# Optimization experiments

Hardware: AMD Instinct MI355X
Metric: run time of the kernel (lower is better)

## Reference

```python
import jax, jax.numpy as jnp
import numpy as np

B, T, D, HD = 256, 256, 384, 64  # batch, seq_len, embedding_dim, head_dim


def setup_inputs() -> dict:
    key = jax.random.key(0)
    k1, k2, k3, k4 = jax.random.split(key, 4)
    x = jax.random.normal(k1, (B, T, D), dtype=jnp.float32)
    # nn.Linear(D, HD, bias=False) weight shape is [HD, D]; init scaled like kaiming-uniform magnitude
    Wq = jax.random.normal(k2, (HD, D), dtype=jnp.float32) * (1.0 / np.sqrt(D))
    Wk = jax.random.normal(k3, (HD, D), dtype=jnp.float32) * (1.0 / np.sqrt(D))
    Wv = jax.random.normal(k4, (HD, D), dtype=jnp.float32) * (1.0 / np.sqrt(D))
    return {"x": x, "Wq": Wq, "Wk": Wk, "Wv": Wv}


def reference(x, Wq, Wk, Wv):
    # Projections: x @ W^T  (Linear with bias=False)
    q = jnp.einsum('btd,hd->bth', x, Wq)  # [B,T,HD]
    k = jnp.einsum('btd,hd->bth', x, Wk)
    v = jnp.einsum('btd,hd->bth', x, Wv)
    scale = 1.0 / np.sqrt(HD).astype(np.float32)
    scores = jnp.einsum('bqh,bkh->bqk', q, k) * scale  # [B,T,T]
    T_ = x.shape[1]
    causal = jnp.tril(jnp.ones((T_, T_), dtype=bool))
    scores = jnp.where(causal, scores, jnp.float32(-jnp.inf))
    attn = jax.nn.softmax(scores, axis=-1)
    # dropout disabled (eval mode) for deterministic reference
    return jnp.einsum('bqk,bkh->bqh', attn, v)
```

## Files before the change

### kernel.cpp

```cpp
#include <hip/hip_runtime.h>

typedef __attribute__((ext_vector_type(8))) short bf16x8;
typedef __attribute__((ext_vector_type(4))) float f32x4;

__device__ inline unsigned short f2bf(float f) {
    unsigned u = __float_as_uint(f);
    return (unsigned short)((u + 0x7fffu + ((u >> 16) & 1u)) >> 16);
}

__global__ void wconv(const float* __restrict__ Wq, const float* __restrict__ Wk,
                      const float* __restrict__ Wv, short* __restrict__ Wcat) {
    int i = blockIdx.x * 256 + threadIdx.x;
    if (i >= 192 * 384) return;
    int row = i / 384;
    int col = i - row * 384;
    const float* src = row < 64 ? (Wq + row * 384)
                     : row < 128 ? (Wk + (row - 64) * 384)
                                 : (Wv + (row - 128) * 384);
    Wcat[i] = (short)f2bf(src[col]);
}

__global__ __launch_bounds__(256) void qkv_proj_mfma(
    const float* __restrict__ x, const short* __restrict__ Wcat,
    short* __restrict__ Qw, short* __restrict__ Kw, short* __restrict__ Vw) {
    __shared__ short xs[128 * 72];
    __shared__ short wsh[192 * 72];
    const int tid = threadIdx.x;
    const int wv = tid >> 6, lane = tid & 63;
    const int g = lane >> 4, c = lane & 15;
    const int wm = (wv >> 1) * 64, wn = (wv & 1) * 96;
    const long long m0 = (long long)blockIdx.x * 128;

    f32x4 acc[4][6];
#pragma unroll
    for (int i = 0; i < 4; ++i)
#pragma unroll
        for (int j = 0; j < 6; ++j) acc[i][j] = (f32x4){0.f, 0.f, 0.f, 0.f};

    for (int kc = 0; kc < 6; ++kc) {
#pragma unroll
        for (int p = 0; p < 8; ++p) {
            int r = p * 16 + (tid >> 4);
            int c4 = tid & 15;
            float4 v = *(const float4*)(x + (m0 + r) * 384 + kc * 64 + c4 * 4);
            unsigned lo = (unsigned)f2bf(v.x) | ((unsigned)f2bf(v.y) << 16);
            unsigned hi = (unsigned)f2bf(v.z) | ((unsigned)f2bf(v.w) << 16);
            *(uint2*)&xs[r * 72 + c4 * 4] = make_uint2(lo, hi);
        }
#pragma unroll
        for (int p = 0; p < 12; ++p) {
            int idx = tid + 256 * p;
            int r = idx >> 4;
            int c2 = idx & 15;
            uint2 w2 = *(const uint2*)(Wcat + r * 384 + kc * 64 + c2 * 4);
            *(uint2*)&wsh[r * 72 + c2 * 4] = w2;
        }
        __syncthreads();
#pragma unroll
        for (int ks = 0; ks < 2; ++ks) {
            bf16x8 af[4], bfr[6];
#pragma unroll
            for (int mi = 0; mi < 4; ++mi)
                af[mi] = *(const bf16x8*)&xs[(wm + 16 * mi + c) * 72 + ks * 32 + g * 8];
#pragma unroll
            for (int nj = 0; nj < 6; ++nj)
                bfr[nj] = *(const bf16x8*)&wsh[(wn + 16 * nj + c) * 72 + ks * 32 + g * 8];
#pragma unroll
            for (int mi = 0; mi < 4; ++mi)
#pragma unroll
                for (int nj = 0; nj < 6; ++nj)
                    acc[mi][nj] = __builtin_amdgcn_mfma_f32_16x16x32_bf16(
                        af[mi], bfr[nj], acc[mi][nj], 0, 0, 0);
        }
        __syncthreads();
    }
#pragma unroll
    for (int mi = 0; mi < 4; ++mi) {
#pragma unroll
        for (int nj = 0; nj < 6; ++nj) {
            int colb = wn + 16 * nj;
            short* dst = colb < 64 ? Qw : (colb < 128 ? Kw : Vw);
            int hc = (colb & 63) + c;
#pragma unroll
            for (int r = 0; r < 4; ++r) {
                long long row = m0 + wm + 16 * mi + 4 * g + r;
                dst[row * 64 + hc] = (short)f2bf(acc[mi][nj][r]);
            }
        }
    }
}

__global__ __launch_bounds__(512) void attn_mfma(
    const short* __restrict__ Qw, const short* __restrict__ Kw,
    const short* __restrict__ Vw, float* __restrict__ out) {
    __shared__ short Ksh[256 * 72];
    __shared__ short Vt[64 * 264];
    __shared__ short Pb[8][16 * 40];
    const int tid = threadIdx.x;
    const int wv = tid >> 6, lane = tid & 63;
    const int g = lane >> 4, c = lane & 15;
    const int b = blockIdx.x;
    const short* Qg = Qw + b * 16384;
    const short* Kg = Kw + b * 16384;
    const short* Vg = Vw + b * 16384;

#pragma unroll
    for (int p = 0; p < 4; ++p) {
        int idx = tid + 512 * p;
        int r = idx >> 3, q8 = idx & 7;
        *(uint4*)&Ksh[r * 72 + q8 * 8] = *(const uint4*)(Kg + r * 64 + q8 * 8);
    }
#pragma unroll
    for (int p = 0; p < 4; ++p) {
        int idx = tid + 512 * p;
        int r = idx >> 3, q8 = idx & 7;
        uint4 v = *(const uint4*)(Vg + r * 64 + q8 * 8);
        unsigned vw[4] = {v.x, v.y, v.z, v.w};
        int swz = (q8 & 7) << 3;
#pragma unroll
        for (int w2 = 0; w2 < 4; ++w2) {
            int h0 = q8 * 8 + w2 * 2;
            Vt[((h0 + 0) * 264 + r) ^ swz] = (short)(vw[w2] & 0xffff);
            Vt[((h0 + 1) * 264 + r) ^ swz] = (short)(vw[w2] >> 16);
        }
    }
    __syncthreads();

    for (int half = 0; half < 2; ++half) {
        const int q0 = (half == 0) ? 16 * wv : 240 - 16 * wv;
        bf16x8 qf0 = *(const bf16x8*)(Qg + (q0 + c) * 64 + g * 8);
        bf16x8 qf1 = *(const bf16x8*)(Qg + (q0 + c) * 64 + 32 + g * 8);
        f32x4 o[4];
#pragma unroll
        for (int nj = 0; nj < 4; ++nj) o[nj] = (f32x4){0.f, 0.f, 0.f, 0.f};
        float m[4] = {-INFINITY, -INFINITY, -INFINITY, -INFINITY};
        float ls[4] = {0.f, 0.f, 0.f, 0.f};
        const int jmax = (q0 + 15) >> 5;

        for (int j = 0; j <= jmax; ++j) {
            f32x4 s0 = {0.f, 0.f, 0.f, 0.f}, s1 = {0.f, 0.f, 0.f, 0.f};
            {
                bf16x8 kf;
                kf = *(const bf16x8*)&Ksh[(32 * j + c) * 72 + g * 8];
                s0 = __builtin_amdgcn_mfma_f32_16x16x32_bf16(qf0, kf, s0, 0, 0, 0);
                kf = *(const bf16x8*)&Ksh[(32 * j + c) * 72 + 32 + g * 8];
                s0 = __builtin_amdgcn_mfma_f32_16x16x32_bf16(qf1, kf, s0, 0, 0, 0);
                kf = *(const bf16x8*)&Ksh[(32 * j + 16 + c) * 72 + g * 8];
                s1 = __builtin_amdgcn_mfma_f32_16x16x32_bf16(qf0, kf, s1, 0, 0, 0);
                kf = *(const bf16x8*)&Ksh[(32 * j + 16 + c) * 72 + 32 + g * 8];
                s1 = __builtin_amdgcn_mfma_f32_16x16x32_bf16(qf1, kf, s1, 0, 0, 0);
            }
            float t0[4], t1[4];
#pragma unroll
            for (int r = 0; r < 4; ++r) {
                t0[r] = s0[r] * 0.125f;
                t1[r] = s1[r] * 0.125f;
            }
            if (j == jmax) {
                int q = q0 + 4 * g;
#pragma unroll
                for (int r = 0; r < 4; ++r) {
                    if (32 * j + c > q + r) t0[r] = -INFINITY;
                    if (32 * j + 16 + c > q + r) t1[r] = -INFINITY;
                }
            }
            float corr[4], p0[4], p1[4];
#pragma unroll
            for (int r = 0; r < 4; ++r) {
                float v = fmaxf(t0[r], t1[r]);
#pragma unroll
                for (int off = 1; off < 16; off <<= 1) v = fmaxf(v, __shfl_xor(v, off, 16));
                float mn = fmaxf(m[r], v);
                corr[r] = __expf(m[r] - mn);
                m[r] = mn;
                p0[r] = __expf(t0[r] - mn);
                p1[r] = __expf(t1[r] - mn);
                float rs = p0[r] + p1[r];
#pragma unroll
                for (int off = 1; off < 16; off <<= 1) rs += __shfl_xor(rs, off, 16);
                ls[r] = ls[r] * corr[r] + rs;
            }
#pragma unroll
            for (int nj = 0; nj < 4; ++nj) {
                f32x4 t = o[nj];
                t[0] *= corr[0]; t[1] *= corr[1]; t[2] *= corr[2]; t[3] *= corr[3];
                o[nj] = t;
            }
            short* pb = Pb[wv];
#pragma unroll
            for (int r = 0; r < 4; ++r) {
                pb[(4 * g + r) * 40 + c]      = (short)f2bf(p0[r]);
                pb[(4 * g + r) * 40 + 16 + c] = (short)f2bf(p1[r]);
            }
            bf16x8 pa = *(const bf16x8*)&pb[c * 40 + g * 8];
#pragma unroll
            for (int nj = 0; nj < 4; ++nj) {
                int h = 16 * nj + c;
                int swz = ((2 * nj + (c >> 3)) & 7) << 3;
                bf16x8 vf = *(const bf16x8*)&Vt[(h * 264 + 32 * j + g * 8) ^ swz];
                o[nj] = __builtin_amdgcn_mfma_f32_16x16x32_bf16(pa, vf, o[nj], 0, 0, 0);
            }
        }
        float inv[4];
#pragma unroll
        for (int r = 0; r < 4; ++r) inv[r] = 1.f / ls[r];
        float* ob = out + ((size_t)b * 256 + q0) * 64;
#pragma unroll
        for (int nj = 0; nj < 4; ++nj)
#pragma unroll
            for (int r = 0; r < 4; ++r)
                ob[(4 * g + r) * 64 + 16 * nj + c] = o[nj][r] * inv[r];
    }
}

extern "C" void kernel_launch(void* const* d_in, const int* in_sizes, int n_in,
                              void* d_out, int out_size, void* d_ws, size_t ws_size,
                              hipStream_t stream) {
    const float* x  = (const float*)d_in[0];
    const float* Wq = (const float*)d_in[1];
    const float* Wk = (const float*)d_in[2];
    const float* Wv = (const float*)d_in[3];
    float* out = (float*)d_out;

    short* Qws  = (short*)d_ws;
    short* Kws  = Qws + (size_t)65536 * 64;
    short* Vws  = Kws + (size_t)65536 * 64;
    short* Wcat = Vws + (size_t)65536 * 64;

    wconv<<<dim3(288), dim3(256), 0, stream>>>(Wq, Wk, Wv, Wcat);
    qkv_proj_mfma<<<dim3(512), dim3(256), 0, stream>>>(x, Wcat, Qws, Kws, Vws);
    attn_mfma<<<dim3(256), dim3(512), 0, stream>>>(Qws, Kws, Vws, out);
}
```

Baseline: 50.76 us.

## Fuse QKV projection into attention kernel, keeping Q/K/V in LDS

Merges the projection GEMM and the attention kernel into one per-batch kernel. Each block computes its 256x192 QKV tile with MFMA, reading x and weight fragments straight from global memory with register prefetch, then writes Q, K and a transposed V into shared memory before running attention. This removes the global round trip for Q/K/V and one kernel launch. In exchange each block does 256 rows of projection with 8 waves, LDS use rises (which may limit occupancy), and the weights are reread per block without LDS staging.

New measurement: 62.75 us. 1.24x slower.

```diff
diff --git a/kernel.cpp b/kernel.cpp
--- a/kernel.cpp
+++ b/kernel.cpp
@@ -20,16 +20,28 @@
     Wcat[i] = (short)f2bf(src[col]);
 }
 
-__global__ __launch_bounds__(256) void qkv_proj_mfma(
+__global__ __launch_bounds__(512, 2) void fused_attn(
     const float* __restrict__ x, const short* __restrict__ Wcat,
-    short* __restrict__ Qw, short* __restrict__ Kw, short* __restrict__ Vw) {
-    __shared__ short xs[128 * 72];
-    __shared__ short wsh[192 * 72];
+    float* __restrict__ out) {
+    __shared__ short Qlds[256 * 72];
+    __shared__ short Ksh[256 * 72];
+    __shared__ short Vt[64 * 264];
+    __shared__ short Pb[8][16 * 40];
+
     const int tid = threadIdx.x;
     const int wv = tid >> 6, lane = tid & 63;
     const int g = lane >> 4, c = lane & 15;
     const int wm = (wv >> 1) * 64, wn = (wv & 1) * 96;
-    const long long m0 = (long long)blockIdx.x * 128;
+    const int b = blockIdx.x;
+
+    const float* xA[4];
+#pragma unroll
+    for (int mi = 0; mi < 4; ++mi)
+        xA[mi] = x + ((size_t)b * 256 + wm + 16 * mi + c) * 384 + g * 8;
+    const short* Bp[6];
+#pragma unroll
+    for (int nj = 0; nj < 6; ++nj)
+        Bp[nj] = Wcat + (wn + 16 * nj + c) * 384 + g * 8;
 
     f32x4 acc[4][6];
 #pragma unroll
@@ -37,99 +49,77 @@
 #pragma unroll
         for (int j = 0; j < 6; ++j) acc[i][j] = (f32x4){0.f, 0.f, 0.f, 0.f};
 
-    for (int kc = 0; kc < 6; ++kc) {
-#pragma unroll
-        for (int p = 0; p < 8; ++p) {
-            int r = p * 16 + (tid >> 4);
-            int c4 = tid & 15;
-            float4 v = *(const float4*)(x + (m0 + r) * 384 + kc * 64 + c4 * 4);
-            unsigned lo = (unsigned)f2bf(v.x) | ((unsigned)f2bf(v.y) << 16);
-            unsigned hi = (unsigned)f2bf(v.z) | ((unsigned)f2bf(v.w) << 16);
-            *(uint2*)&xs[r * 72 + c4 * 4] = make_uint2(lo, hi);
-        }
-#pragma unroll
-        for (int p = 0; p < 12; ++p) {
-            int idx = tid + 256 * p;
-            int r = idx >> 4;
-            int c2 = idx & 15;
-            uint2 w2 = *(const uint2*)(Wcat + r * 384 + kc * 64 + c2 * 4);
-            *(uint2*)&wsh[r * 72 + c2 * 4] = w2;
-        }
-        __syncthreads();
-#pragma unroll
-        for (int ks = 0; ks < 2; ++ks) {
-            bf16x8 af[4], bfr[6];
-#pragma unroll
-            for (int mi = 0; mi < 4; ++mi)
-                af[mi] = *(const bf16x8*)&xs[(wm + 16 * mi + c) * 72 + ks * 32 + g * 8];
+    float4 pa[4][2];
+#pragma unroll
+    for (int mi = 0; mi < 4; ++mi) {
+        pa[mi][0] = *(const float4*)(xA[mi] + 0);
+        pa[mi][1] = *(const float4*)(xA[mi] + 4);
+    }
+
+    for (int s = 0; s < 12; ++s) {
+        const int kn = (s < 11 ? s + 1 : 11) * 32;
+        float4 na[4][2];
+#pragma unroll
+        for (int mi = 0; mi < 4; ++mi) {
+            na[mi][0] = *(const float4*)(xA[mi] + kn + 0);
+            na[mi][1] = *(const float4*)(xA[mi] + kn + 4);
+        }
+        bf16x8 bfr[6];
+#pragma unroll
+        for (int nj = 0; nj < 6; ++nj)
+            bfr[nj] = *(const bf16x8*)(Bp[nj] + s * 32);
+        bf16x8 af[4];
+#pragma unroll
+        for (int mi = 0; mi < 4; ++mi) {
+            bf16x8 t;
+            t[0] = (short)f2bf(pa[mi][0].x); t[1] = (short)f2bf(pa[mi][0].y);
+            t[2] = (short)f2bf(pa[mi][0].z); t[3] = (short)f2bf(pa[mi][0].w);
+            t[4] = (short)f2bf(pa[mi][1].x); t[5] = (short)f2bf(pa[mi][1].y);
+            t[6] = (short)f2bf(pa[mi][1].z); t[7] = (short)f2bf(pa[mi][1].w);
+            af[mi] = t;
+        }
+#pragma unroll
+        for (int mi = 0; mi < 4; ++mi)
 #pragma unroll
             for (int nj = 0; nj < 6; ++nj)
-                bfr[nj] = *(const bf16x8*)&wsh[(wn + 16 * nj + c) * 72 + ks * 32 + g * 8];
-#pragma unroll
-            for (int mi = 0; mi < 4; ++mi)
-#pragma unroll
-                for (int nj = 0; nj < 6; ++nj)
-                    acc[mi][nj] = __builtin_amdgcn_mfma_f32_16x16x32_bf16(
-                        af[mi], bfr[nj], acc[mi][nj], 0, 0, 0);
-        }
-        __syncthreads();
-    }
+                acc[mi][nj] = __builtin_amdgcn_mfma_f32_16x16x32_bf16(
+                    af[mi], bfr[nj], acc[mi][nj], 0, 0, 0);
+#pragma unroll
+        for (int mi = 0; mi < 4; ++mi) {
+            pa[mi][0] = na[mi][0];
+            pa[mi][1] = na[mi][1];
+        }
+    }
+
 #pragma unroll
     for (int mi = 0; mi < 4; ++mi) {
 #pragma unroll
         for (int nj = 0; nj < 6; ++nj) {
-            int colb = wn + 16 * nj;
-            short* dst = colb < 64 ? Qw : (colb < 128 ? Kw : Vw);
-            int hc = (colb & 63) + c;
-#pragma unroll
-            for (int r = 0; r < 4; ++r) {
-                long long row = m0 + wm + 16 * mi + 4 * g + r;
-                dst[row * 64 + hc] = (short)f2bf(acc[mi][nj][r]);
-            }
-        }
-    }
-}
-
-__global__ __launch_bounds__(512) void attn_mfma(
-    const short* __restrict__ Qw, const short* __restrict__ Kw,
-    const short* __restrict__ Vw, float* __restrict__ out) {
-    __shared__ short Ksh[256 * 72];
-    __shared__ short Vt[64 * 264];
-    __shared__ short Pb[8][16 * 40];
-    const int tid = threadIdx.x;
-    const int wv = tid >> 6, lane = tid & 63;
-    const int g = lane >> 4, c = lane & 15;
-    const int b = blockIdx.x;
-    const short* Qg = Qw + b * 16384;
-    const short* Kg = Kw + b * 16384;
-    const short* Vg = Vw + b * 16384;
-
-#pragma unroll
-    for (int p = 0; p < 4; ++p) {
-        int idx = tid + 512 * p;
-        int r = idx >> 3, q8 = idx & 7;
-        *(uint4*)&Ksh[r * 72 + q8 * 8] = *(const uint4*)(Kg + r * 64 + q8 * 8);
-    }
-#pragma unroll
-    for (int p = 0; p < 4; ++p) {
-        int idx = tid + 512 * p;
-        int r = idx >> 3, q8 = idx & 7;
-        uint4 v = *(const uint4*)(Vg + r * 64 + q8 * 8);
-        unsigned vw[4] = {v.x, v.y, v.z, v.w};
-        int swz = (q8 & 7) << 3;
-#pragma unroll
-        for (int w2 = 0; w2 < 4; ++w2) {
-            int h0 = q8 * 8 + w2 * 2;
-            Vt[((h0 + 0) * 264 + r) ^ swz] = (short)(vw[w2] & 0xffff);
-            Vt[((h0 + 1) * 264 + r) ^ swz] = (short)(vw[w2] >> 16);
+            const int colb = wn + 16 * nj;
+            const int row = wm + 16 * mi + 4 * g;
+            if (colb < 64) {
+#pragma unroll
+                for (int r = 0; r < 4; ++r)
+                    Qlds[(row + r) * 72 + colb + c] = (short)f2bf(acc[mi][nj][r]);
+            } else if (colb < 128) {
+#pragma unroll
+                for (int r = 0; r < 4; ++r)
+                    Ksh[(row + r) * 72 + (colb - 64) + c] = (short)f2bf(acc[mi][nj][r]);
+            } else {
+                const int h = colb - 128 + c;
+                const int swz = ((h >> 3) & 7) << 3;
+#pragma unroll
+                for (int r = 0; r < 4; ++r)
+                    Vt[(h * 264 + row + r) ^ swz] = (short)f2bf(acc[mi][nj][r]);
+            }
         }
     }
     __syncthreads();
 
     for (int half = 0; half < 2; ++half) {
         const int q0 = (half == 0) ? 16 * wv : 240 - 16 * wv;
-        bf16x8 qf0 = *(const bf16x8*)(Qg + (q0 + c) * 64 + g * 8);
-        bf16x8 qf1 = *(const bf16x8*)(Qg + (q0 + c) * 64 + 32 + g * 8);
+        bf16x8 qf0 = *(const bf16x8*)&Qlds[(q0 + c) * 72 + g * 8];
+        bf16x8 qf1 = *(const bf16x8*)&Qlds[(q0 + c) * 72 + 32 + g * 8];
         f32x4 o[4];
 #pragma unroll
         for (int nj = 0; nj < 4; ++nj) o[nj] = (f32x4){0.f, 0.f, 0.f, 0.f};
@@ -192,13 +182,13 @@
                 pb[(4 * g + r) * 40 + c]      = (short)f2bf(p0[r]);
                 pb[(4 * g + r) * 40 + 16 + c] = (short)f2bf(p1[r]);
             }
-            bf16x8 pa = *(const bf16x8*)&pb[c * 40 + g * 8];
+            bf16x8 pfa = *(const bf16x8*)&pb[c * 40 + g * 8];
 #pragma unroll
             for (int nj = 0; nj < 4; ++nj) {
                 int h = 16 * nj + c;
                 int swz = ((2 * nj + (c >> 3)) & 7) << 3;
                 bf16x8 vf = *(const bf16x8*)&Vt[(h * 264 + 32 * j + g * 8) ^ swz];
-                o[nj] = __builtin_amdgcn_mfma_f32_16x16x32_bf16(pa, vf, o[nj], 0, 0, 0);
+                o[nj] = __builtin_amdgcn_mfma_f32_16x16x32_bf16(pfa, vf, o[nj], 0, 0, 0);
             }
         }
         float inv[4];
@@ -222,12 +212,8 @@
     const float* Wv = (const float*)d_in[3];
     float* out = (float*)d_out;
 
-    short* Qws  = (short*)d_ws;
-    short* Kws  = Qws + (size_t)65536 * 64;
-    short* Vws  = Kws + (size_t)65536 * 64;
-    short* Wcat = Vws + (size_t)65536 * 64;
+    short* Wcat = (short*)d_ws;
 
     wconv<<<dim3(288), dim3(256), 0, stream>>>(Wq, Wk, Wv, Wcat);
-    qkv_proj_mfma<<<dim3(512), dim3(256), 0, stream>>>(x, Wcat, Qws, Kws, Vws);
-    attn_mfma<<<dim3(256), dim3(512), 0, stream>>>(Qws, Kws, Vws, out);
-}
+    fused_attn<<<dim3(256), dim3(512), 0, stream>>>(x, Wcat, out);
+}
```

## Double-buffer QKV projection with direct global-to-LDS loads and pre-swizzled weights

Applied to the files above, without the earlier changes.

The projection kernel now stages x (as fp32) and a pre-packed, XOR-swizzled bf16 weight layout straight into LDS with global_load_lds. The two LDS buffers are alternated so the load of the next 32-wide K chunk overlaps the MFMAs on the current one. The fp32-to-bf16 conversion of x moves to after the LDS read, and outputs go through an LDS staging tile so Q/K/V are written with 16-byte coalesced stores. Launch bounds now ask for 2 blocks per CU, which adds register pressure, and the K loop now runs 12 iterations with a barrier in each.

Result: faster. 47.03 us (-7.4%).

```diff
diff --git a/kernel.cpp b/kernel.cpp
--- a/kernel.cpp
+++ b/kernel.cpp
@@ -8,28 +8,39 @@
     return (unsigned short)((u + 0x7fffu + ((u >> 16) & 1u)) >> 16);
 }
 
+__device__ inline void gload16(const void* g, void* l) {
+    __builtin_amdgcn_global_load_lds(
+        (const __attribute__((address_space(1))) unsigned*)g,
+        (__attribute__((address_space(3))) unsigned*)l, 16, 0, 0);
+}
+
 __global__ void wconv(const float* __restrict__ Wq, const float* __restrict__ Wk,
-                      const float* __restrict__ Wv, short* __restrict__ Wcat) {
+                      const float* __restrict__ Wv, short* __restrict__ Wp) {
     int i = blockIdx.x * 256 + threadIdx.x;
     if (i >= 192 * 384) return;
-    int row = i / 384;
-    int col = i - row * 384;
-    const float* src = row < 64 ? (Wq + row * 384)
-                     : row < 128 ? (Wk + (row - 64) * 384)
-                                 : (Wv + (row - 128) * 384);
-    Wcat[i] = (short)f2bf(src[col]);
-}
-
-__global__ __launch_bounds__(256) void qkv_proj_mfma(
-    const float* __restrict__ x, const short* __restrict__ Wcat,
+    int col = i / 384;
+    int k   = i - col * 384;
+    const float* src = col < 64 ? (Wq + col * 384)
+                     : col < 128 ? (Wk + (col - 64) * 384)
+                                 : (Wv + (col - 128) * 384);
+    int kc = k >> 5, g = (k >> 3) & 3, kl = k & 7;
+    Wp[kc * 6144 + (((g * 192 + col) ^ g) << 3) + kl] = (short)f2bf(src[k]);
+}
+
+__global__ __launch_bounds__(256, 2) void qkv_proj(
+    const float* __restrict__ x, const short* __restrict__ Wp,
     short* __restrict__ Qw, short* __restrict__ Kw, short* __restrict__ Vw) {
-    __shared__ short xs[128 * 72];
-    __shared__ short wsh[192 * 72];
+    __shared__ unsigned char LDSRAW[57344];
+    float* const xb0 = (float*)LDSRAW;
+    float* const xb1 = xb0 + 4096;
+    short* const wb0 = (short*)(LDSRAW + 32768);
+    short* const wb1 = wb0 + 6144;
+
     const int tid = threadIdx.x;
     const int wv = tid >> 6, lane = tid & 63;
     const int g = lane >> 4, c = lane & 15;
     const int wm = (wv >> 1) * 64, wn = (wv & 1) * 96;
-    const long long m0 = (long long)blockIdx.x * 128;
+    const size_t m0 = (size_t)blockIdx.x * 128;
 
     f32x4 acc[4][6];
 #pragma unroll
@@ -37,65 +48,96 @@
 #pragma unroll
         for (int j = 0; j < 6; ++j) acc[i][j] = (f32x4){0.f, 0.f, 0.f, 0.f};
 
-    for (int kc = 0; kc < 6; ++kc) {
-#pragma unroll
-        for (int p = 0; p < 8; ++p) {
-            int r = p * 16 + (tid >> 4);
-            int c4 = tid & 15;
-            float4 v = *(const float4*)(x + (m0 + r) * 384 + kc * 64 + c4 * 4);
-            unsigned lo = (unsigned)f2bf(v.x) | ((unsigned)f2bf(v.y) << 16);
-            unsigned hi = (unsigned)f2bf(v.z) | ((unsigned)f2bf(v.w) << 16);
-            *(uint2*)&xs[r * 72 + c4 * 4] = make_uint2(lo, hi);
-        }
-#pragma unroll
-        for (int p = 0; p < 12; ++p) {
-            int idx = tid + 256 * p;
-            int r = idx >> 4;
-            int c2 = idx & 15;
-            uint2 w2 = *(const uint2*)(Wcat + r * 384 + kc * 64 + c2 * 4);
-            *(uint2*)&wsh[r * 72 + c2 * 4] = w2;
-        }
+    const int xrow8 = lane >> 3;
+    const int xgcol = ((lane & 7) ^ xrow8) << 2;
+
+#define STAGE_X(KC, XB)                                                       \
+    {                                                                         \
+        _Pragma("unroll")                                                     \
+        for (int i_ = 0; i_ < 4; ++i_) {                                      \
+            int seg = wv * 4 + i_;                                            \
+            const float* gp = x + (m0 + seg * 8 + xrow8) * 384 + (KC) * 32 + xgcol; \
+            gload16(gp, (XB) + seg * 256);                                    \
+        }                                                                     \
+    }
+#define STAGE_W(KC, WB)                                                       \
+    {                                                                         \
+        _Pragma("unroll")                                                     \
+        for (int i_ = 0; i_ < 3; ++i_) {                                      \
+            int seg = wv * 3 + i_;                                            \
+            const short* gp = Wp + (KC) * 6144 + seg * 512 + lane * 8;        \
+            gload16(gp, (WB) + seg * 512);                                    \
+        }                                                                     \
+    }
+
+    STAGE_X(0, xb0)
+    STAGE_W(0, wb0)
+    asm volatile("s_waitcnt vmcnt(0)" ::: "memory");
+    __syncthreads();
+
+    for (int s = 0; s < 12; ++s) {
+        if (s < 11) {
+            if (s & 1) { STAGE_X(s + 1, xb0) STAGE_W(s + 1, wb0) }
+            else       { STAGE_X(s + 1, xb1) STAGE_W(s + 1, wb1) }
+        }
+        const float* xb = (s & 1) ? xb1 : xb0;
+        const short* wb = (s & 1) ? wb1 : wb0;
+        bf16x8 af[4], bfr[6];
+#pragma unroll
+        for (int mi = 0; mi < 4; ++mi) {
+            const int row = wm + 16 * mi + c;
+            const int rx = row & 7;
+            f32x4 lo = *(const f32x4*)&xb[row * 32 + (((2 * g) ^ rx) << 2)];
+            f32x4 hi = *(const f32x4*)&xb[row * 32 + (((2 * g + 1) ^ rx) << 2)];
+            bf16x8 t;
+            t[0] = (short)f2bf(lo[0]); t[1] = (short)f2bf(lo[1]);
+            t[2] = (short)f2bf(lo[2]); t[3] = (short)f2bf(lo[3]);
+            t[4] = (short)f2bf(hi[0]); t[5] = (short)f2bf(hi[1]);
+            t[6] = (short)f2bf(hi[2]); t[7] = (short)f2bf(hi[3]);
+            af[mi] = t;
+        }
+#pragma unroll
+        for (int nj = 0; nj < 6; ++nj)
+            bfr[nj] = *(const bf16x8*)&wb[((g * 192 + wn + 16 * nj + c) ^ g) << 3];
+#pragma unroll
+        for (int mi = 0; mi < 4; ++mi)
+#pragma unroll
+            for (int nj = 0; nj < 6; ++nj)
+                acc[mi][nj] = __builtin_amdgcn_mfma_f32_16x16x32_bf16(
+                    af[mi], bfr[nj], acc[mi][nj], 0, 0, 0);
+        asm volatile("s_waitcnt vmcnt(0)" ::: "memory");
         __syncthreads();
-#pragma unroll
-        for (int ks = 0; ks < 2; ++ks) {
-            bf16x8 af[4], bfr[6];
-#pragma unroll
-            for (int mi = 0; mi < 4; ++mi)
-                af[mi] = *(const bf16x8*)&xs[(wm + 16 * mi + c) * 72 + ks * 32 + g * 8];
-#pragma unroll
-            for (int nj = 0; nj < 6; ++nj)
-                bfr[nj] = *(const bf16x8*)&wsh[(wn + 16 * nj + c) * 72 + ks * 32 + g * 8];
-#pragma unroll
-            for (int mi = 0; mi < 4; ++mi)
-#pragma unroll
-                for (int nj = 0; nj < 6; ++nj)
-                    acc[mi][nj] = __builtin_amdgcn_mfma_f32_16x16x32_bf16(
-                        af[mi], bfr[nj], acc[mi][nj], 0, 0, 0);
-        }
-        __syncthreads();
-    }
-#pragma unroll
-    for (int mi = 0; mi < 4; ++mi) {
+    }
+
+    short* ep = (short*)LDSRAW;
+#pragma unroll
+    for (int mi = 0; mi < 4; ++mi)
 #pragma unroll
         for (int nj = 0; nj < 6; ++nj) {
-            int colb = wn + 16 * nj;
-            short* dst = colb < 64 ? Qw : (colb < 128 ? Kw : Vw);
-            int hc = (colb & 63) + c;
-#pragma unroll
-            for (int r = 0; r < 4; ++r) {
-                long long row = m0 + wm + 16 * mi + 4 * g + r;
-                dst[row * 64 + hc] = (short)f2bf(acc[mi][nj][r]);
-            }
-        }
-    }
-}
-
-__global__ __launch_bounds__(512) void attn_mfma(
+            const int row = wm + 16 * mi + 4 * g;
+#pragma unroll
+            for (int r = 0; r < 4; ++r)
+                ep[(row + r) * 192 + wn + 16 * nj + c] = (short)f2bf(acc[mi][nj][r]);
+        }
+    __syncthreads();
+#pragma unroll
+    for (int p = 0; p < 4; ++p) {
+        int u = tid + 256 * p;
+        int row = u >> 3, c8 = u & 7;
+        *(uint4*)(Qw + (m0 + row) * 64 + c8 * 8) = *(const uint4*)&ep[row * 192 + c8 * 8];
+        *(uint4*)(Kw + (m0 + row) * 64 + c8 * 8) = *(const uint4*)&ep[row * 192 + 64 + c8 * 8];
+        *(uint4*)(Vw + (m0 + row) * 64 + c8 * 8) = *(const uint4*)&ep[row * 192 + 128 + c8 * 8];
+    }
+#undef STAGE_X
+#undef STAGE_W
+}
+
+__global__ __launch_bounds__(512, 2) void attn_mfma(
     const short* __restrict__ Qw, const short* __restrict__ Kw,
     const short* __restrict__ Vw, float* __restrict__ out) {
     __shared__ short Ksh[256 * 72];
     __shared__ short Vt[64 * 264];
-    __shared__ short Pb[8][16 * 40];
+    __shared__ short Pb[8][640];
     const int tid = threadIdx.x;
     const int wv = tid >> 6, lane = tid & 63;
     const int g = lane >> 4, c = lane & 15;
@@ -192,13 +234,13 @@
                 pb[(4 * g + r) * 40 + c]      = (short)f2bf(p0[r]);
                 pb[(4 * g + r) * 40 + 16 + c] = (short)f2bf(p1[r]);
             }
-            bf16x8 pa = *(const bf16x8*)&pb[c * 40 + g * 8];
+            bf16x8 pfa = *(const bf16x8*)&pb[c * 40 + g * 8];
 #pragma unroll
             for (int nj = 0; nj < 4; ++nj) {
                 int h = 16 * nj + c;
                 int swz = ((2 * nj + (c >> 3)) & 7) << 3;
                 bf16x8 vf = *(const bf16x8*)&Vt[(h * 264 + 32 * j + g * 8) ^ swz];
-                o[nj] = __builtin_amdgcn_mfma_f32_16x16x32_bf16(pa, vf, o[nj], 0, 0, 0);
+                o[nj] = __builtin_amdgcn_mfma_f32_16x16x32_bf16(pfa, vf, o[nj], 0, 0, 0);
             }
         }
         float inv[4];
@@ -222,12 +264,12 @@
     const float* Wv = (const float*)d_in[3];
     float* out = (float*)d_out;
 
-    short* Qws  = (short*)d_ws;
-    short* Kws  = Qws + (size_t)65536 * 64;
-    short* Vws  = Kws + (size_t)65536 * 64;
-    short* Wcat = Vws + (size_t)65536 * 64;
-
-    wconv<<<dim3(288), dim3(256), 0, stream>>>(Wq, Wk, Wv, Wcat);
-    qkv_proj_mfma<<<dim3(512), dim3(256), 0, stream>>>(x, Wcat, Qws, Kws, Vws);
+    short* Qws = (short*)d_ws;
+    short* Kws = Qws + (size_t)65536 * 64;
+    short* Vws = Kws + (size_t)65536 * 64;
+    short* Wp  = Vws + (size_t)65536 * 64;
+
+    wconv<<<dim3(288), dim3(256), 0, stream>>>(Wq, Wk, Wv, Wp);
+    qkv_proj<<<dim3(512), dim3(256), 0, stream>>>(x, Wp, Qws, Kws, Vws);
     attn_mfma<<<dim3(256), dim3(512), 0, stream>>>(Qws, Kws, Vws, out);
 }
```
